# Optimization experiments

Hardware: AMD Instinct MI355X
Metric: run time of the kernel (lower is better)

Reference implementation:

```python
import jax, jax.numpy as jnp
import numpy as np

DIM = 1024
G = 256            # group_size
QK = 128           # query_key_dim
HID = 2048         # int(dim * expansion_factor)
NUM_BUCKETS = 32
MAX_DIST = 128
BIAS_SCALE = QK ** 0.5
LN_EPS = 1e-5


def t5_rel_bias(rel_table):
    # causal T5 relative position bias for a [G, G] block
    pos = jnp.arange(G)
    rel = pos[None, :] - pos[:, None]          # k_pos - q_pos
    n = jnp.maximum(-rel, 0)                   # causal clamp
    max_exact = NUM_BUCKETS // 2               # 16
    is_small = n < max_exact
    ln_ratio = np.log(MAX_DIST / max_exact)
    val_large = max_exact + (
        jnp.log(jnp.maximum(n, 1).astype(jnp.float32) / max_exact) / ln_ratio
        * (NUM_BUCKETS - max_exact)
    ).astype(jnp.int32)
    val_large = jnp.minimum(val_large, NUM_BUCKETS - 1)
    bucket = jnp.where(is_small, n, val_large)
    return rel_table[bucket] * BIAS_SCALE      # [G, G]


def setup_inputs() -> dict:
    key = jax.random.key(0)
    ks = jax.random.split(key, 10)
    s = 0.02
    return {
        "x": jax.random.normal(ks[0], (4, 4096, DIM), dtype=jnp.float32),
        "ln_w": jnp.ones((DIM,), jnp.float32),
        "ln_b": jnp.zeros((DIM,), jnp.float32),
        "Wh": jax.random.normal(ks[1], (DIM, 2 * HID), jnp.float32) * s,
        "bh": jnp.zeros((2 * HID,), jnp.float32),
        "Wqk": jax.random.normal(ks[2], (DIM, QK), jnp.float32) * s,
        "bqk": jnp.zeros((QK,), jnp.float32),
        "qk_w": jax.random.normal(ks[3], (4, QK), jnp.float32) * s + 1.0,
        "qk_b": jnp.zeros((4, QK), jnp.float32),
        "rel_table": jax.random.normal(ks[4], (NUM_BUCKETS,), jnp.float32) * s,
        "Wout": jax.random.normal(ks[5], (HID, DIM), jnp.float32) * s,
        "bout": jnp.zeros((DIM,), jnp.float32),
    }


def reference(x, ln_w, ln_b, Wh, bh, Wqk, bqk, qk_w, qk_b, rel_table, Wout, bout):
    b, n, _ = x.shape
    g = G
    ng = n // g

    # LayerNorm
    mu = jnp.mean(x, -1, keepdims=True)
    var = jnp.var(x, -1, keepdims=True)
    normed = (x - mu) * jax.lax.rsqrt(var + LN_EPS) * ln_w + ln_b

    # projections
    hv = jax.nn.silu(normed @ Wh + bh)
    v, gate = jnp.split(hv, 2, axis=-1)                 # [b, n, HID] each
    qk = jax.nn.silu(normed @ Wqk + bqk)                # [b, n, QK]

    # offset-scale into 4 heads
    qk4 = qk[..., None, :] * qk_w + qk_b                # [b, n, 4, QK]
    quad_q, lin_q, quad_k, lin_k = [qk4[..., h, :] for h in range(4)]

    # group: b (g n) d -> b g n d
    grp = lambda t: t.reshape(b, ng, g, t.shape[-1])
    quad_q, quad_k, lin_q, lin_k, vg = map(grp, (quad_q, quad_k, lin_q, lin_k, v))

    # quadratic branch: ReLU^2 attention with T5 bias, causal within group
    sim = jnp.einsum('bgid,bgjd->bgij', quad_q, quad_k) / g
    sim = sim + t5_rel_bias(rel_table)
    attn = jnp.square(jax.nn.relu(sim))
    causal_mask = jnp.triu(jnp.ones((g, g), bool), 1)
    attn = jnp.where(causal_mask, 0.0, attn)
    quad_out = jnp.einsum('bgij,bgje->bgie', attn, vg)  # [b, ng, g, HID]

    # linear branch: per-group kv summary, causal via shifted cumsum over groups
    lin_kv = jnp.einsum('bgnd,bgne->bgde', lin_k, vg) / g   # [b, ng, QK, HID]
    lin_kv = jnp.cumsum(lin_kv, axis=1)
    lin_kv = jnp.pad(lin_kv, ((0, 0), (1, 0), (0, 0), (0, 0)))[:, :-1]
    lin_out = jnp.einsum('bgde,bgnd->bgne', lin_kv, lin_q)  # [b, ng, g, HID]

    out = gate * (quad_out + lin_out).reshape(b, n, HID)
    return out @ Wout + bout + x
```

## Files before the change

kernel.cpp:

```cpp
#include <hip/hip_runtime.h>
#include <hip/hip_bf16.h>

typedef unsigned short u16;
typedef short s8v __attribute__((ext_vector_type(8)));
typedef float f4v __attribute__((ext_vector_type(4)));

__device__ __forceinline__ float b2f(u16 u) { return __uint_as_float(((unsigned)u) << 16); }
__device__ __forceinline__ u16 f2b(float f) {
    unsigned u = __float_as_uint(f);
    unsigned r = 0x7FFFu + ((u >> 16) & 1u);
    return (u16)((u + r) >> 16);
}
__device__ __forceinline__ float silu_f(float x) { return x / (1.0f + expf(-x)); }

__device__ __forceinline__ void gld16(const u16* g, u16* l) {
    __builtin_amdgcn_global_load_lds((const __attribute__((address_space(1))) unsigned*)g,
                                     (__attribute__((address_space(3))) unsigned*)l, 16, 0, 0);
}

__device__ __forceinline__ void mfma_block(const u16* Al, const u16* Bl, f4v acc[4][4],
                                           int wr, int wc, int l15, int quad, int l7) {
#pragma unroll
    for (int ks = 0; ks < 2; ++ks) {
        s8v af[4], bf[4];
        int cch = ((ks * 4 + quad) ^ l7) * 8;
#pragma unroll
        for (int mi = 0; mi < 4; ++mi)
            af[mi] = *(const s8v*)(Al + (wr * 64 + mi * 16 + l15) * 64 + cch);
#pragma unroll
        for (int ni = 0; ni < 4; ++ni)
            bf[ni] = *(const s8v*)(Bl + (wc * 64 + ni * 16 + l15) * 64 + cch);
#pragma unroll
        for (int mi = 0; mi < 4; ++mi)
#pragma unroll
            for (int ni = 0; ni < 4; ++ni)
                acc[mi][ni] = __builtin_amdgcn_mfma_f32_16x16x32_bf16(af[mi], bf[ni], acc[mi][ni], 0, 0, 0);
    }
}

__device__ __forceinline__ void stage_plane(const u16* __restrict__ src, int K, int kbase,
                                            u16* dst, int t) {
    const int row = t >> 2, ch = t & 3;
    const int csw = (ch ^ (row & 3) ^ ((row >> 2) & 3)) * 8;
    gld16(src + (size_t)row * K + kbase + csw, dst + row * 32 + ch * 8);
    gld16(src + (size_t)(row + 128) * K + kbase + csw, dst + (row + 128) * 32 + ch * 8);
}

__device__ __forceinline__ void read_frag4(const u16* plane, s8v (&f)[4], int rbase, int l15, int quad) {
#pragma unroll
    for (int mi = 0; mi < 4; ++mi) {
        int r = rbase + mi * 16 + l15;
        f[mi] = *(const s8v*)(plane + r * 32 + ((quad ^ (r & 3) ^ ((r >> 2) & 3)) * 8));
    }
}

__device__ __forceinline__ void kloop2ph(const u16* __restrict__ Ag, const u16* __restrict__ Bg,
                                         int K, int NT, u16* lds8, f4v (&acc)[8][4],
                                         int t, int wm, int wn, int l15, int quad) {
#pragma unroll
    for (int T = 0; T < 3; ++T) {
        u16* Ab = lds8 + T * 16384;
        stage_plane(Ag, K, T * 32, Ab, t);
        stage_plane(Bg, K, T * 32, Ab + 8192, t);
    }
    asm volatile("s_waitcnt vmcnt(8)" ::: "memory");
    __builtin_amdgcn_s_barrier();

    s8v bf[4];
    for (int T = 0; T < NT; ++T) {
        const u16* Ab = lds8 + (T & 3) * 16384;
        const u16* Bb = Ab + 8192;
        u16* Sb = lds8 + ((T + 3) & 3) * 16384;
        const bool st = (T < NT - 3);
        s8v af[4];
        read_frag4(Bb, bf, wn * 64, l15, quad);
        read_frag4(Ab, af, wm * 128, l15, quad);
        if (st) stage_plane(Ag, K, (T + 3) * 32, Sb, t);
        __builtin_amdgcn_s_setprio(1);
#pragma unroll
        for (int mi = 0; mi < 4; ++mi)
#pragma unroll
            for (int ni = 0; ni < 4; ++ni)
                acc[mi][ni] = __builtin_amdgcn_mfma_f32_16x16x32_bf16(af[mi], bf[ni], acc[mi][ni], 0, 0, 0);
        __builtin_amdgcn_s_setprio(0);
        __builtin_amdgcn_s_barrier();
        read_frag4(Ab, af, wm * 128 + 64, l15, quad);
        if (st) stage_plane(Bg, K, (T + 3) * 32, Sb + 8192, t);
        __builtin_amdgcn_s_setprio(1);
#pragma unroll
        for (int mi = 0; mi < 4; ++mi)
#pragma unroll
            for (int ni = 0; ni < 4; ++ni)
                acc[4 + mi][ni] = __builtin_amdgcn_mfma_f32_16x16x32_bf16(af[mi], bf[ni], acc[4 + mi][ni], 0, 0, 0);
        __builtin_amdgcn_s_setprio(0);
        if (T < NT - 3)       asm volatile("s_waitcnt vmcnt(8)" ::: "memory");
        else if (T == NT - 3) asm volatile("s_waitcnt vmcnt(4)" ::: "memory");
        else if (T == NT - 2) asm volatile("s_waitcnt vmcnt(0)" ::: "memory");
        __builtin_amdgcn_s_barrier();
    }
}


__global__ __launch_bounds__(256) void convT_all(const float* __restrict__ Wh,
                                                 const float* __restrict__ Wout,
                                                 const float* __restrict__ Wqk,
                                                 u16* __restrict__ WhT,
                                                 u16* __restrict__ WoutT,
                                                 u16* __restrict__ WqkT) {
    __shared__ float tile[32][33];
    int b = blockIdx.x;
    const float* in; u16* out; int K, N, bx, by;
    if (b < 4096)      { in = Wh;   out = WhT;   K = 1024; N = 4096; bx = b & 127; by = b >> 7; }
    else if (b < 6144) { b -= 4096; in = Wout; out = WoutT; K = 2048; N = 1024; bx = b & 31; by = b >> 5; }
    else               { b -= 6144; in = Wqk;  out = WqkT;  K = 1024; N = 128;  bx = b & 3;  by = b >> 2; }
    int k0 = by * 32, n0 = bx * 32;
    int t = threadIdx.x;
    int r = t >> 5, c = t & 31;
#pragma unroll
    for (int rr = r; rr < 32; rr += 8) tile[rr][c] = in[(size_t)(k0 + rr) * N + n0 + c];
    __syncthreads();
#pragma unroll
    for (int rr = r; rr < 32; rr += 8) out[(size_t)(n0 + rr) * K + k0 + c] = f2b(tile[c][rr]);
}

__global__ __launch_bounds__(256) void ln_kernel(const float* __restrict__ x,
                                                 const float* __restrict__ w,
                                                 const float* __restrict__ bsh,
                                                 u16* __restrict__ out) {
    int row = blockIdx.x, t = threadIdx.x;
    const float* xr = x + (size_t)row * 1024;
    float4 u = *reinterpret_cast<const float4*>(xr + t * 4);
    float s = u.x + u.y + u.z + u.w;
    float s2 = u.x * u.x + u.y * u.y + u.z * u.z + u.w * u.w;
#pragma unroll
    for (int o = 32; o; o >>= 1) {
        s += __shfl_down(s, o, 64);
        s2 += __shfl_down(s2, o, 64);
    }
    __shared__ float rs[4], rs2[4];
    int wid = t >> 6;
    if ((t & 63) == 0) { rs[wid] = s; rs2[wid] = s2; }
    __syncthreads();
    float S = rs[0] + rs[1] + rs[2] + rs[3];
    float S2 = rs2[0] + rs2[1] + rs2[2] + rs2[3];
    float mu = S * (1.0f / 1024.0f);
    float var = S2 * (1.0f / 1024.0f) - mu * mu;
    float rinv = rsqrtf(var + 1e-5f);
    float4 uw = *reinterpret_cast<const float4*>(w + t * 4);
    float4 ub = *reinterpret_cast<const float4*>(bsh + t * 4);
    ushort4 o;
    o.x = f2b((u.x - mu) * rinv * uw.x + ub.x);
    o.y = f2b((u.y - mu) * rinv * uw.y + ub.y);
    o.z = f2b((u.z - mu) * rinv * uw.z + ub.z);
    o.w = f2b((u.w - mu) * rinv * uw.w + ub.w);
    *reinterpret_cast<ushort4*>(out + (size_t)row * 1024 + t * 4) = o;
}

__global__ __launch_bounds__(512) void gemm_hv256(const u16* __restrict__ A,
                                                  const u16* __restrict__ Bt,
                                                  const float* __restrict__ bias,
                                                  u16* __restrict__ vT,
                                                  u16* __restrict__ gate) {
    __shared__ __align__(16) u16 lds8[65536];
    const int t = threadIdx.x;
    const int lane = t & 63, w = t >> 6;
    const int wm = w >> 2, wn = w & 3;
    const int l15 = lane & 15, quad = lane >> 4;

    int wg = blockIdx.x;
    wg = (wg & 7) * 128 + (wg >> 3);
    const int by = wg >> 4, bx = wg & 15;
    const int m0 = by * 256, n0 = bx * 256;

    f4v acc[8][4] = {};
    kloop2ph(A + (size_t)m0 * 1024, Bt + (size_t)n0 * 1024, 1024, 32,
             lds8, acc, t, wm, wn, l15, quad);

    const bool isV = (n0 < 2048);
    const int bg = by;
#pragma unroll
    for (int ni = 0; ni < 4; ++ni) {
        int n = n0 + wn * 64 + ni * 16 + l15;
        float bs = bias[n];
#pragma unroll
        for (int mi = 0; mi < 8; ++mi) {
            int mloc = wm * 128 + mi * 16 + quad * 4;
            if (isV) {
                ushort4 o;
                o.x = f2b(silu_f(acc[mi][ni][0] + bs));
                o.y = f2b(silu_f(acc[mi][ni][1] + bs));
                o.z = f2b(silu_f(acc[mi][ni][2] + bs));
                o.w = f2b(silu_f(acc[mi][ni][3] + bs));
                *reinterpret_cast<ushort4*>(vT + ((size_t)bg * 2048 + n) * 256 + mloc) = o;
            } else {
#pragma unroll
                for (int reg = 0; reg < 4; ++reg)
                    gate[(size_t)(m0 + mloc + reg) * 2048 + (n - 2048)] =
                        f2b(silu_f(acc[mi][ni][reg] + bs));
            }
        }
    }
}

__global__ __launch_bounds__(512) void gemm_out256(const u16* __restrict__ A,
                                                   const u16* __restrict__ Bt,
                                                   const float* __restrict__ bias,
                                                   const float* __restrict__ resid,
                                                   float* __restrict__ C) {
    __shared__ __align__(16) u16 lds8[65536];
    const int t = threadIdx.x;
    const int lane = t & 63, w = t >> 6;
    const int wm = w >> 2, wn = w & 3;
    const int l15 = lane & 15, quad = lane >> 4;

    int wg = blockIdx.x;
    wg = (wg & 7) * 32 + (wg >> 3);
    const int by = wg >> 2, bx = wg & 3;
    const int m0 = by * 256, n0 = bx * 256;

    f4v acc[8][4] = {};
    kloop2ph(A + (size_t)m0 * 2048, Bt + (size_t)n0 * 2048, 2048, 64,
             lds8, acc, t, wm, wn, l15, quad);

#pragma unroll
    for (int ni = 0; ni < 4; ++ni) {
        int n = n0 + wn * 64 + ni * 16 + l15;
        float bs = bias[n];
#pragma unroll
        for (int mi = 0; mi < 8; ++mi) {
#pragma unroll
            for (int reg = 0; reg < 4; ++reg) {
                int m = m0 + wm * 128 + mi * 16 + quad * 4 + reg;
                C[(size_t)m * 1024 + n] = acc[mi][ni][reg] + bs + resid[(size_t)m * 1024 + n];
            }
        }
    }
}

__global__ __launch_bounds__(256) void gemm_qk(const u16* __restrict__ A,
                                               const u16* __restrict__ Bt,
                                               const float* __restrict__ bias,
                                               const float* __restrict__ qk_w,
                                               const float* __restrict__ qk_b,
                                               u16* __restrict__ C,
                                               u16* __restrict__ klT) {
    __shared__ __align__(16) u16 Al[128 * 64];
    __shared__ __align__(16) u16 Bl[128 * 64];
    const int t = threadIdx.x;
    const int lane = t & 63, w = t >> 6;
    const int wr = w >> 1, wc = w & 1;
    const int l15 = lane & 15, quad = lane >> 4, l7 = lane & 7;
    const int m0 = blockIdx.y * 128;
    const int sr = t >> 3, ss = t & 7;

    f4v acc[4][4] = {};
    for (int k0 = 0; k0 < 1024; k0 += 64) {
#pragma unroll
        for (int i = 0; i < 4; ++i) {
            int r = i * 32 + sr;
            int q = ss ^ (r & 7);
            gld16(A + (size_t)(m0 + r) * 1024 + q * 8 + k0, Al + i * 2048 + t * 8);
            gld16(Bt + (size_t)r * 1024 + q * 8 + k0, Bl + i * 2048 + t * 8);
        }
        __syncthreads();
        mfma_block(Al, Bl, acc, wr, wc, l15, quad, l7);
        __syncthreads();
    }
#pragma unroll
    for (int ni = 0; ni < 4; ++ni) {
        int n = wc * 64 + ni * 16 + l15;
        float bs = bias[n];
        float kw = qk_w[3 * 128 + n], kb = qk_b[3 * 128 + n];
#pragma unroll
        for (int mi = 0; mi < 4; ++mi) {
#pragma unroll
            for (int reg = 0; reg < 4; ++reg) {
                int m = m0 + wr * 64 + mi * 16 + quad * 4 + reg;
                u16 qv = f2b(silu_f(acc[mi][ni][reg] + bs));
                C[(size_t)m * 128 + n] = qv;
                klT[(((size_t)(m >> 8)) * 128 + n) * 256 + (m & 255)] = f2b(b2f(qv) * kw + kb);
            }
        }
    }
}

__global__ __launch_bounds__(256) void scores_kernel(const u16* __restrict__ qk,
                                                     const float* __restrict__ qk_w,
                                                     const float* __restrict__ qk_b,
                                                     const float* __restrict__ rel_table,
                                                     u16* __restrict__ Sbuf) {
    __shared__ __align__(16) u16 qkl[256 * 128];
    __shared__ float biasn[256];
    __shared__ float w0[128], b0[128], w1[128], b1[128], w2[128], b2v[128];
    const int t = threadIdx.x;
    const int bg = blockIdx.x >> 1, mt = blockIdx.x & 1;
    const int lane = t & 63, w = t >> 6;
    const int wr = w >> 1, wc = w & 1;
    const int l15 = lane & 15, quad = lane >> 4;

    if (t < 128) {
        w0[t] = qk_w[t];        b0[t] = qk_b[t];
        w1[t] = qk_w[128 + t];  b1[t] = qk_b[128 + t];
        w2[t] = qk_w[256 + t];  b2v[t] = qk_b[256 + t];
    }
    {
        int n = t;
        int bucket;
        if (n < 16) bucket = n;
        else {
            float v = logf((float)n / 16.0f) / 2.0794415416798357f * 16.0f;
            int vl = 16 + (int)v;
            bucket = vl > 31 ? 31 : vl;
        }
        biasn[n] = rel_table[bucket] * 11.313708498984761f;
    }
#pragma unroll
    for (int it = 0; it < 16; ++it) {
        int r = (t >> 4) + it * 16, c = (t & 15) * 8;
        *(s8v*)(qkl + r * 128 + c) = *(const s8v*)(qk + ((size_t)(bg * 256 + r)) * 128 + c);
    }
    __syncthreads();

    f4v acc[4][8] = {};
#pragma unroll
    for (int kstep = 0; kstep < 4; ++kstep) {
        int kc = kstep * 32 + quad * 8;
        float w0f[8], b0f[8], w2f[8], b2f_[8];
#pragma unroll
        for (int j = 0; j < 8; ++j) {
            w0f[j] = w0[kc + j]; b0f[j] = b0[kc + j];
            w2f[j] = w2[kc + j]; b2f_[j] = b2v[kc + j];
        }
        s8v af[4];
#pragma unroll
        for (int mi = 0; mi < 4; ++mi) {
            int ra = mt * 128 + wr * 64 + mi * 16 + l15;
            s8v raw = *(const s8v*)(qkl + ra * 128 + kc);
#pragma unroll
            for (int j = 0; j < 8; ++j) af[mi][j] = (short)f2b(b2f((u16)raw[j]) * w0f[j] + b0f[j]);
        }
#pragma unroll
        for (int np = 0; np < 2; ++np) {
            s8v bf[4];
#pragma unroll
            for (int ni = 0; ni < 4; ++ni) {
                int rb = wc * 128 + (np * 4 + ni) * 16 + l15;
                s8v raw = *(const s8v*)(qkl + rb * 128 + kc);
#pragma unroll
                for (int j = 0; j < 8; ++j) bf[ni][j] = (short)f2b(b2f((u16)raw[j]) * w2f[j] + b2f_[j]);
            }
#pragma unroll
            for (int mi = 0; mi < 4; ++mi)
#pragma unroll
                for (int ni = 0; ni < 4; ++ni)
                    acc[mi][np * 4 + ni] = __builtin_amdgcn_mfma_f32_16x16x32_bf16(af[mi], bf[ni], acc[mi][np * 4 + ni], 0, 0, 0);
        }
    }
#pragma unroll
    for (int ni = 0; ni < 8; ++ni) {
        int gj = wc * 128 + ni * 16 + l15;
#pragma unroll
        for (int mi = 0; mi < 4; ++mi) {
#pragma unroll
            for (int reg = 0; reg < 4; ++reg) {
                int gi = mt * 128 + wr * 64 + mi * 16 + quad * 4 + reg;
                float aval = 0.0f;
                if (gj <= gi) {
                    float sv = acc[mi][ni][reg] * (1.0f / 256.0f) + biasn[gi - gj];
                    sv = fmaxf(sv, 0.0f);
                    aval = sv * sv;
                }
                Sbuf[((size_t)bg * 256 + gi) * 384 + gj] = f2b(aval);
            }
        }
    }
#pragma unroll
    for (int it = 0; it < 8; ++it) {
        int i = mt * 128 + (t >> 4) + it * 16;
        int d = (t & 15) * 8;
        s8v raw = *(const s8v*)(qkl + i * 128 + d);
        u16* dst = Sbuf + ((size_t)bg * 256 + i) * 384 + 256 + d;
#pragma unroll
        for (int j = 0; j < 8; ++j)
            dst[j] = f2b(b2f((u16)raw[j]) * w1[d + j] + b1[d + j]);
    }
}

__global__ __launch_bounds__(256) void kv_gemm(const u16* __restrict__ vT,
                                               const u16* __restrict__ klT,
                                               u16* __restrict__ kvT) {
    __shared__ __align__(16) u16 Al[128 * 64];
    __shared__ __align__(16) u16 Bl[128 * 64];
    const int t = threadIdx.x;
    const int lane = t & 63, w = t >> 6;
    const int wr = w >> 1, wc = w & 1;
    const int l15 = lane & 15, quad = lane >> 4, l7 = lane & 7;
    const int bg = blockIdx.y, m0 = blockIdx.x * 128;
    const int sr = t >> 3, ss = t & 7;

    const u16* Av = vT + (size_t)bg * 2048 * 256;
    const u16* Bk = klT + (size_t)bg * 128 * 256;

    f4v acc[4][4] = {};
    for (int k0 = 0; k0 < 256; k0 += 64) {
#pragma unroll
        for (int i = 0; i < 4; ++i) {
            int r = i * 32 + sr;
            int q = ss ^ (r & 7);
            gld16(Av + (size_t)(m0 + r) * 256 + q * 8 + k0, Al + i * 2048 + t * 8);
            gld16(Bk + (size_t)r * 256 + q * 8 + k0, Bl + i * 2048 + t * 8);
        }
        __syncthreads();
        mfma_block(Al, Bl, acc, wr, wc, l15, quad, l7);
        __syncthreads();
    }
#pragma unroll
    for (int ni = 0; ni < 4; ++ni) {
        int n = wc * 64 + ni * 16 + l15;
#pragma unroll
        for (int mi = 0; mi < 4; ++mi) {
#pragma unroll
            for (int reg = 0; reg < 4; ++reg) {
                int m = m0 + wr * 64 + mi * 16 + quad * 4 + reg;
                kvT[((size_t)bg * 2048 + m) * 128 + n] = f2b(acc[mi][ni][reg] * (1.0f / 256.0f));
            }
        }
    }
}

__global__ __launch_bounds__(256) void prefix_kernel(u16* __restrict__ kvT) {
    size_t tid = (size_t)blockIdx.x * 256 + threadIdx.x;
    int d = (int)(tid & 127);
    int e = (int)((tid >> 7) & 2047);
    int b = (int)(tid >> 18);
    size_t base = ((size_t)(b * 16) * 2048 + e) * 128 + d;
    const size_t gs = 2048 * 128;
    float vals[16];
#pragma unroll
    for (int g = 0; g < 16; ++g) vals[g] = b2f(kvT[base + (size_t)g * gs]);
    float s = 0.0f;
#pragma unroll
    for (int g = 0; g < 16; ++g) {
        kvT[base + (size_t)g * gs] = f2b(s);
        s += vals[g];
    }
}

__global__ __launch_bounds__(256) void attn_gemm(const u16* __restrict__ Sbuf,
                                                 const u16* __restrict__ vT,
                                                 const u16* __restrict__ kvT,
                                                 u16* __restrict__ gate) {
    __shared__ __align__(16) u16 Al[128 * 64];
    __shared__ __align__(16) u16 Bl[128 * 64];
    const int t = threadIdx.x;
    const int lane = t & 63, w = t >> 6;
    const int wr = w >> 1, wc = w & 1;
    const int l15 = lane & 15, quad = lane >> 4, l7 = lane & 7;
    const int bg = blockIdx.y >> 1, mt = blockIdx.y & 1;
    const int n0 = blockIdx.x * 128;
    const int sr = t >> 3, ss = t & 7;

    const u16* Abase = Sbuf + ((size_t)bg * 256 + mt * 128) * 384;
    const u16* Bv = vT + (size_t)bg * 2048 * 256;
    const u16* Bk = kvT + (size_t)bg * 2048 * 128;

    f4v acc[4][4] = {};
    for (int k0 = 0; k0 < 256; k0 += 64) {
#pragma unroll
        for (int i = 0; i < 4; ++i) {
            int r = i * 32 + sr;
            int q = ss ^ (r & 7);
            gld16(Abase + (size_t)r * 384 + q * 8 + k0, Al + i * 2048 + t * 8);
            gld16(Bv + (size_t)(n0 + r) * 256 + q * 8 + k0, Bl + i * 2048 + t * 8);
        }
        __syncthreads();
        mfma_block(Al, Bl, acc, wr, wc, l15, quad, l7);
        __syncthreads();
    }
    for (int k0 = 0; k0 < 128; k0 += 64) {
#pragma unroll
        for (int i = 0; i < 4; ++i) {
            int r = i * 32 + sr;
            int q = ss ^ (r & 7);
            gld16(Abase + (size_t)r * 384 + 256 + q * 8 + k0, Al + i * 2048 + t * 8);
            gld16(Bk + (size_t)(n0 + r) * 128 + q * 8 + k0, Bl + i * 2048 + t * 8);
        }
        __syncthreads();
        mfma_block(Al, Bl, acc, wr, wc, l15, quad, l7);
        __syncthreads();
    }
#pragma unroll
    for (int ni = 0; ni < 4; ++ni) {
        int e = n0 + wc * 64 + ni * 16 + l15;
#pragma unroll
        for (int mi = 0; mi < 4; ++mi) {
#pragma unroll
            for (int reg = 0; reg < 4; ++reg) {
                int gi = mt * 128 + wr * 64 + mi * 16 + quad * 4 + reg;
                u16* p = gate + ((size_t)bg * 256 + gi) * 2048 + e;
                *p = f2b(acc[mi][ni][reg] * b2f(*p));
            }
        }
    }
}

extern "C" void kernel_launch(void* const* d_in, const int* in_sizes, int n_in,
                              void* d_out, int out_size, void* d_ws, size_t ws_size,
                              hipStream_t stream) {
    const float* x = (const float*)d_in[0];
    const float* ln_w = (const float*)d_in[1];
    const float* ln_b = (const float*)d_in[2];
    const float* Wh = (const float*)d_in[3];
    const float* bh = (const float*)d_in[4];
    const float* Wqk = (const float*)d_in[5];
    const float* bqk = (const float*)d_in[6];
    const float* qk_w = (const float*)d_in[7];
    const float* qk_b = (const float*)d_in[8];
    const float* rel_table = (const float*)d_in[9];
    const float* Wout = (const float*)d_in[10];
    const float* bout = (const float*)d_in[11];
    float* out = (float*)d_out;

    char* ws = (char*)d_ws;
    u16* normed = (u16*)(ws);
    u16* kvT    = (u16*)(ws);
    u16* gate   = (u16*)(ws + 33554432ull);
    u16* vT     = (u16*)(ws + 100663296ull);
    u16* qk     = (u16*)(ws + 167772160ull);
    u16* WhT    = (u16*)(ws + 171966464ull);
    u16* klT    = (u16*)(ws + 171966464ull);
    u16* WoutT  = (u16*)(ws + 180355072ull);
    u16* Sbuf   = (u16*)(ws + 184549376ull);
    u16* WqkT   = (u16*)(ws + 184549376ull);

    convT_all<<<6272, 256, 0, stream>>>(Wh, Wout, Wqk, WhT, WoutT, WqkT);
    ln_kernel<<<16384, 256, 0, stream>>>(x, ln_w, ln_b, normed);
    gemm_hv256<<<1024, 512, 0, stream>>>(normed, WhT, bh, vT, gate);
    gemm_qk<<<dim3(1, 128), 256, 0, stream>>>(normed, WqkT, bqk, qk_w, qk_b, qk, klT);
    scores_kernel<<<128, 256, 0, stream>>>(qk, qk_w, qk_b, rel_table, Sbuf);
    kv_gemm<<<dim3(16, 64), 256, 0, stream>>>(vT, klT, kvT);
    prefix_kernel<<<4096, 256, 0, stream>>>(kvT);
    attn_gemm<<<dim3(16, 128), 256, 0, stream>>>(Sbuf, vT, kvT, gate);
    gemm_out256<<<256, 512, 0, stream>>>(gate, WoutT, bout, x, out);
}
```

Measured before the change: 574.1 us.

## Port attn_gemm to 256x256 tiles using pipelined kloop2ph with strided operands

Generalizes the pipelined k-loop helper to take separate row strides for A and B. Rewrites attn_gemm to use 512-thread blocks computing 256x256 output tiles via two kloop2ph passes (score×V and score×prefix-KV), replacing the 128x128 synchronous loop. This aims to increase operand reuse and overlap global loads with MFMA. The risk is that the short K (12 steps total) leaves pipeline fill and drain exposed, and the grid shrinks to 512 blocks.

```diff
diff --git a/kernel.cpp b/kernel.cpp
--- a/kernel.cpp
+++ b/kernel.cpp
@@ -54,14 +54,15 @@
     }
 }
 
-__device__ __forceinline__ void kloop2ph(const u16* __restrict__ Ag, const u16* __restrict__ Bg,
-                                         int K, int NT, u16* lds8, f4v (&acc)[8][4],
+__device__ __forceinline__ void kloop2ph(const u16* __restrict__ Ag, int sA,
+                                         const u16* __restrict__ Bg, int sB,
+                                         int NT, u16* lds8, f4v (&acc)[8][4],
                                          int t, int wm, int wn, int l15, int quad) {
 #pragma unroll
     for (int T = 0; T < 3; ++T) {
         u16* Ab = lds8 + T * 16384;
-        stage_plane(Ag, K, T * 32, Ab, t);
-        stage_plane(Bg, K, T * 32, Ab + 8192, t);
+        stage_plane(Ag, sA, T * 32, Ab, t);
+        stage_plane(Bg, sB, T * 32, Ab + 8192, t);
     }
     asm volatile("s_waitcnt vmcnt(8)" ::: "memory");
     __builtin_amdgcn_s_barrier();
@@ -75,7 +76,7 @@
         s8v af[4];
         read_frag4(Bb, bf, wn * 64, l15, quad);
         read_frag4(Ab, af, wm * 128, l15, quad);
-        if (st) stage_plane(Ag, K, (T + 3) * 32, Sb, t);
+        if (st) stage_plane(Ag, sA, (T + 3) * 32, Sb, t);
         __builtin_amdgcn_s_setprio(1);
 #pragma unroll
         for (int mi = 0; mi < 4; ++mi)
@@ -85,7 +86,7 @@
         __builtin_amdgcn_s_setprio(0);
         __builtin_amdgcn_s_barrier();
         read_frag4(Ab, af, wm * 128 + 64, l15, quad);
-        if (st) stage_plane(Bg, K, (T + 3) * 32, Sb + 8192, t);
+        if (st) stage_plane(Bg, sB, (T + 3) * 32, Sb + 8192, t);
         __builtin_amdgcn_s_setprio(1);
 #pragma unroll
         for (int mi = 0; mi < 4; ++mi)
@@ -173,7 +174,7 @@
     const int m0 = by * 256, n0 = bx * 256;
 
     f4v acc[8][4] = {};
-    kloop2ph(A + (size_t)m0 * 1024, Bt + (size_t)n0 * 1024, 1024, 32,
+    kloop2ph(A + (size_t)m0 * 1024, 1024, Bt + (size_t)n0 * 1024, 1024, 32,
              lds8, acc, t, wm, wn, l15, quad);
 
     const bool isV = (n0 < 2048);
@@ -219,7 +220,7 @@
     const int m0 = by * 256, n0 = bx * 256;
 
     f4v acc[8][4] = {};
-    kloop2ph(A + (size_t)m0 * 2048, Bt + (size_t)n0 * 2048, 2048, 64,
+    kloop2ph(A + (size_t)m0 * 2048, 2048, Bt + (size_t)n0 * 2048, 2048, 64,
              lds8, acc, t, wm, wn, l15, quad);
 
 #pragma unroll
@@ -446,57 +447,34 @@
     }
 }
 
-__global__ __launch_bounds__(256) void attn_gemm(const u16* __restrict__ Sbuf,
+__global__ __launch_bounds__(512) void attn_gemm(const u16* __restrict__ Sbuf,
                                                  const u16* __restrict__ vT,
                                                  const u16* __restrict__ kvT,
                                                  u16* __restrict__ gate) {
-    __shared__ __align__(16) u16 Al[128 * 64];
-    __shared__ __align__(16) u16 Bl[128 * 64];
+    __shared__ __align__(16) u16 lds8[65536];
     const int t = threadIdx.x;
     const int lane = t & 63, w = t >> 6;
-    const int wr = w >> 1, wc = w & 1;
-    const int l15 = lane & 15, quad = lane >> 4, l7 = lane & 7;
-    const int bg = blockIdx.y >> 1, mt = blockIdx.y & 1;
-    const int n0 = blockIdx.x * 128;
-    const int sr = t >> 3, ss = t & 7;
-
-    const u16* Abase = Sbuf + ((size_t)bg * 256 + mt * 128) * 384;
-    const u16* Bv = vT + (size_t)bg * 2048 * 256;
-    const u16* Bk = kvT + (size_t)bg * 2048 * 128;
-
-    f4v acc[4][4] = {};
-    for (int k0 = 0; k0 < 256; k0 += 64) {
-#pragma unroll
-        for (int i = 0; i < 4; ++i) {
-            int r = i * 32 + sr;
-            int q = ss ^ (r & 7);
-            gld16(Abase + (size_t)r * 384 + q * 8 + k0, Al + i * 2048 + t * 8);
-            gld16(Bv + (size_t)(n0 + r) * 256 + q * 8 + k0, Bl + i * 2048 + t * 8);
-        }
-        __syncthreads();
-        mfma_block(Al, Bl, acc, wr, wc, l15, quad, l7);
-        __syncthreads();
-    }
-    for (int k0 = 0; k0 < 128; k0 += 64) {
-#pragma unroll
-        for (int i = 0; i < 4; ++i) {
-            int r = i * 32 + sr;
-            int q = ss ^ (r & 7);
-            gld16(Abase + (size_t)r * 384 + 256 + q * 8 + k0, Al + i * 2048 + t * 8);
-            gld16(Bk + (size_t)(n0 + r) * 128 + q * 8 + k0, Bl + i * 2048 + t * 8);
-        }
-        __syncthreads();
-        mfma_block(Al, Bl, acc, wr, wc, l15, quad, l7);
-        __syncthreads();
-    }
+    const int wm = w >> 2, wn = w & 3;
+    const int l15 = lane & 15, quad = lane >> 4;
+    const int bg = blockIdx.y;
+    const int n0 = blockIdx.x * 256;
+
+    const u16* Aa = Sbuf + (size_t)bg * 256 * 384;
+    const u16* Bv = vT + (size_t)bg * 2048 * 256 + (size_t)n0 * 256;
+    const u16* Bk = kvT + (size_t)bg * 2048 * 128 + (size_t)n0 * 128;
+
+    f4v acc[8][4] = {};
+    kloop2ph(Aa, 384, Bv, 256, 8, lds8, acc, t, wm, wn, l15, quad);
+    kloop2ph(Aa + 256, 384, Bk, 128, 4, lds8, acc, t, wm, wn, l15, quad);
+
 #pragma unroll
     for (int ni = 0; ni < 4; ++ni) {
-        int e = n0 + wc * 64 + ni * 16 + l15;
-#pragma unroll
-        for (int mi = 0; mi < 4; ++mi) {
+        int e = n0 + wn * 64 + ni * 16 + l15;
+#pragma unroll
+        for (int mi = 0; mi < 8; ++mi) {
 #pragma unroll
             for (int reg = 0; reg < 4; ++reg) {
-                int gi = mt * 128 + wr * 64 + mi * 16 + quad * 4 + reg;
+                int gi = wm * 128 + mi * 16 + quad * 4 + reg;
                 u16* p = gate + ((size_t)bg * 256 + gi) * 2048 + e;
                 *p = f2b(acc[mi][ni][reg] * b2f(*p));
             }
@@ -540,6 +518,6 @@
     scores_kernel<<<128, 256, 0, stream>>>(qk, qk_w, qk_b, rel_table, Sbuf);
     kv_gemm<<<dim3(16, 64), 256, 0, stream>>>(vT, klT, kvT);
     prefix_kernel<<<4096, 256, 0, stream>>>(kvT);
-    attn_gemm<<<dim3(16, 128), 256, 0, stream>>>(Sbuf, vT, kvT, gate);
+    attn_gemm<<<dim3(8, 64), 512, 0, stream>>>(Sbuf, vT, kvT, gate);
     gemm_out256<<<256, 512, 0, stream>>>(gate, WoutT, bout, x, out);
 }
```

Result: slower. 603.9 us (+5.2%).
